# Optimization experiments

Measured on AMD Instinct MI355X. Metric: run time of the kernel, lower is better.

Reference implementation:

```python
import jax, jax.numpy as jnp
import numpy as np


def _axis_taps(g, size):
    # g: continuous grid coordinate; returns two neighbor indices (clamped)
    # and their linear interpolation weights, matching the HDRNet CUDA kernel:
    #   w = max(1 - |i + 0.5 - g|, 0)
    f = jnp.floor(g - 0.5)
    taps = []
    for off in (0.0, 1.0):
        idx = f + off
        w = jnp.maximum(1.0 - jnp.abs(idx + 0.5 - g), 0.0)
        i = jnp.clip(idx, 0, size - 1).astype(jnp.int32)
        taps.append((i, w))
    return taps


def bilateral_slice_apply(grid, guide, inp):
    # grid: [B, gh, gw, gd, n_out*(n_in+1)]   (has_offset=True)
    # guide: [B, H, W] in [0,1]
    # inp:  [B, H, W, n_in]
    B, gh, gw, gd, nc = grid.shape
    _, H, W, n_in = inp.shape
    n_out = nc // (n_in + 1)

    # continuous grid coords for each pixel / guide value
    gx = (jnp.arange(W, dtype=grid.dtype) + 0.5) * (gw / W)   # [W]
    gy = (jnp.arange(H, dtype=grid.dtype) + 0.5) * (gh / H)   # [H]
    gz = guide * gd                                           # [B,H,W]

    x_taps = _axis_taps(gx, gw)   # idx/w: [W]
    y_taps = _axis_taps(gy, gh)   # idx/w: [H]
    z_taps = _axis_taps(gz, gd)   # idx/w: [B,H,W]

    b = jnp.arange(B)[:, None, None]
    coeff = jnp.zeros((B, H, W, nc), dtype=grid.dtype)
    for yi, wy in y_taps:
        for xi, wx in x_taps:
            for zi, wz in z_taps:
                g = grid[b, yi[None, :, None], xi[None, None, :], zi]  # [B,H,W,nc]
                w = (wy[None, :, None] * wx[None, None, :] * wz)[..., None]
                coeff = coeff + w * g

    # per-pixel affine apply: out_o = sum_i A[o,i]*in_i + A[o,n_in]
    coeff = coeff.reshape(B, H, W, n_out, n_in + 1)
    out = jnp.einsum('bhwoc,bhwc->bhwo', coeff[..., :n_in], inp) + coeff[..., n_in]
    return out


def setup_inputs() -> dict:
    key = jax.random.key(0)
    k1, k2, k3 = jax.random.split(key, 3)
    B, gh, gw, gd = 4, 16, 16, 8
    H, W, n_in, n_out = 1024, 1024, 3, 3
    nc = n_out * (n_in + 1)  # has_offset=True -> 12
    grid = jax.random.normal(k1, (B, gh, gw, gd, nc), dtype=jnp.float32)
    guide = jax.random.uniform(k2, (B, H, W), dtype=jnp.float32)
    inp = jax.random.normal(k3, (B, H, W, n_in), dtype=jnp.float32)
    return {"grid": grid, "guide": guide, "input": inp}


def reference(grid, guide, input):
    return bilateral_slice_apply(grid, guide, input)
```

## Files before the change

### kernel.cpp

```cpp
#include <hip/hip_runtime.h>


__global__ __launch_bounds__(256) void BilateralSliceApply_kernel(
    const float* __restrict__ grid,
    const float* __restrict__ guide,
    const float* __restrict__ inp,
    float* __restrict__ out)
{
    __shared__ float4 lxi[3072];

    const int tx = blockIdx.x;
    const int ty = blockIdx.y;
    const int b  = blockIdx.z;
    const int t  = threadIdx.x;
    const int xl = t & 63;

    const int x0 = tx << 6;
    const int y0 = ty << 5;

    const int fy  = (ty == 0) ? -1 : ((ty - 1) >> 1);
    const int ycA = fy < 0 ? 0 : fy;
    const int ycB = (fy + 1 > 15) ? 15 : fy + 1;

    const int fx  = (xl < 32) ? (tx - 1) : tx;
    const int ix0 = fx < 0 ? 0 : fx;
    const int ix1 = (fx + 1 > 15) ? 15 : fx + 1;
    const float wx1 = ((float)(x0 + xl) + 0.5f) * 0.015625f - 0.5f - (float)fx;

    const int bbase = b << 4;
    for (int i = t >> 6; i < 48; i += 4) {
        const int z  = i & 7;
        const int w  = i >> 3;
        const int yc = (w >= 3) ? 1 : 0;
        const int c4 = w - yc * 3;
        const int ycell = yc ? ycB : ycA;
        const int cb = (bbase + ycell) << 4;
        const float* g0 = grid + ((size_t)(((cb + ix0) << 3) + z) * 12 + (c4 << 2));
        const float* g1 = grid + ((size_t)(((cb + ix1) << 3) + z) * 12 + (c4 << 2));
        const float4 a  = *(const float4*)g0;
        const float4 c  = *(const float4*)g1;
        float4 v;
        v.x = fmaf(wx1, c.x - a.x, a.x);
        v.y = fmaf(wx1, c.y - a.y, a.y);
        v.z = fmaf(wx1, c.z - a.z, a.z);
        v.w = fmaf(wx1, c.w - a.w, a.w);
        lxi[((((yc << 3) + z) * 3 + c4) << 6) + xl] = v;
    }
    __syncthreads();

    const int r0 = t >> 6;
#pragma unroll 2
    for (int k = 0; k < 8; ++k) {
        const int row = r0 + (k << 2);
        const int y   = y0 + row;
        const float wy1 = ((float)y + 0.5f) * 0.015625f - 0.5f - (float)fy;
        const float wy0 = 1.0f - wy1;
        const int pp = (((b << 10) + y) << 10) + x0 + xl;

        const float gz  = guide[pp] * 8.0f;
        const float fz  = floorf(gz - 0.5f);
        const float wz1 = gz - 0.5f - fz;
        const float wz0 = 1.0f - wz1;
        const int ifz = (int)fz;
        const int iz0 = ifz < 0 ? 0 : (ifz > 7 ? 7 : ifz);
        const int nz  = ifz + 1;
        const int iz1 = nz < 0 ? 0 : (nz > 7 ? 7 : nz);

        const float wA0 = wy0 * wz0, wA1 = wy0 * wz1;
        const float wB0 = wy1 * wz0, wB1 = wy1 * wz1;

        const int bA0 = ((iz0 * 3) << 6) + xl;
        const int bA1 = ((iz1 * 3) << 6) + xl;
        const int bB0 = (((8 + iz0) * 3) << 6) + xl;
        const int bB1 = (((8 + iz1) * 3) << 6) + xl;

        float4 cc[3];
#pragma unroll
        for (int c4 = 0; c4 < 3; ++c4) {
            const int o = c4 << 6;
            const float4 vA0 = lxi[bA0 + o];
            const float4 vA1 = lxi[bA1 + o];
            const float4 vB0 = lxi[bB0 + o];
            const float4 vB1 = lxi[bB1 + o];
            float4 v;
            v.x = fmaf(wA0, vA0.x, fmaf(wA1, vA1.x, fmaf(wB0, vB0.x, wB1 * vB1.x)));
            v.y = fmaf(wA0, vA0.y, fmaf(wA1, vA1.y, fmaf(wB0, vB0.y, wB1 * vB1.y)));
            v.z = fmaf(wA0, vA0.z, fmaf(wA1, vA1.z, fmaf(wB0, vB0.z, wB1 * vB1.z)));
            v.w = fmaf(wA0, vA0.w, fmaf(wA1, vA1.w, fmaf(wB0, vB0.w, wB1 * vB1.w)));
            cc[c4] = v;
        }

        const float in0 = inp[pp * 3 + 0];
        const float in1 = inp[pp * 3 + 1];
        const float in2 = inp[pp * 3 + 2];

        out[pp * 3 + 0] = fmaf(cc[0].x, in0, fmaf(cc[0].y, in1, fmaf(cc[0].z, in2, cc[0].w)));
        out[pp * 3 + 1] = fmaf(cc[1].x, in0, fmaf(cc[1].y, in1, fmaf(cc[1].z, in2, cc[1].w)));
        out[pp * 3 + 2] = fmaf(cc[2].x, in0, fmaf(cc[2].y, in1, fmaf(cc[2].z, in2, cc[2].w)));
    }
}

extern "C" void kernel_launch(void* const* d_in, const int* in_sizes, int n_in,
                              void* d_out, int out_size, void* d_ws, size_t ws_size,
                              hipStream_t stream) {
    const float* grid  = (const float*)d_in[0];
    const float* guide = (const float*)d_in[1];
    const float* inp   = (const float*)d_in[2];
    float* out = (float*)d_out;

    dim3 gridDim(16, 32, 4);
    BilateralSliceApply_kernel<<<gridDim, 256, 0, stream>>>(grid, guide, inp, out);
}
```

Measured before the change: 130.1 us.

## Store x-interpolated grid in fp16 shared memory and blend with packed half2 math

Stores the x-interpolated grid coefficients in shared memory as half2 pairs instead of float4, halving the LDS footprint and the bytes read per pixel. Each thread now loads all 12 channels per cell row in one pass, and the yz trilinear blend runs as packed half2 FMAs. Launch bounds now request 6 waves per SIMD and the unroll-2 pragma is removed. The tradeoff is reduced accuracy from fp16 storage and accumulation, which may exceed tolerance.

Measured after the change: 117.6 us. -9.6%, faster.

```diff
diff --git a/kernel.cpp b/kernel.cpp
--- a/kernel.cpp
+++ b/kernel.cpp
@@ -1,13 +1,18 @@
 #include <hip/hip_runtime.h>
+#include <hip/hip_fp16.h>
 
 
-__global__ __launch_bounds__(256) void BilateralSliceApply_kernel(
+struct __align__(16) H2x4 { __half2 x, y, z, w; };
+struct __align__(8)  H2x2 { __half2 a, b; };
+
+__global__ __launch_bounds__(256, 6) void BilateralSliceApply_kernel(
     const float* __restrict__ grid,
     const float* __restrict__ guide,
     const float* __restrict__ inp,
     float* __restrict__ out)
 {
-    __shared__ float4 lxi[3072];
+    __shared__ H2x4 lA[1024];
+    __shared__ H2x4 lB[512];
 
     const int tx = blockIdx.x;
     const int ty = blockIdx.y;
@@ -28,28 +33,50 @@
     const float wx1 = ((float)(x0 + xl) + 0.5f) * 0.015625f - 0.5f - (float)fx;
 
     const int bbase = b << 4;
-    for (int i = t >> 6; i < 48; i += 4) {
-        const int z  = i & 7;
-        const int w  = i >> 3;
-        const int yc = (w >= 3) ? 1 : 0;
-        const int c4 = w - yc * 3;
+    const int g0grp = t >> 6;
+#pragma unroll
+    for (int q = 0; q < 4; ++q) {
+        const int L  = g0grp + (q << 2);
+        const int yc = L >> 3;
+        const int z  = L & 7;
         const int ycell = yc ? ycB : ycA;
         const int cb = (bbase + ycell) << 4;
-        const float* g0 = grid + ((size_t)(((cb + ix0) << 3) + z) * 12 + (c4 << 2));
-        const float* g1 = grid + ((size_t)(((cb + ix1) << 3) + z) * 12 + (c4 << 2));
-        const float4 a  = *(const float4*)g0;
-        const float4 c  = *(const float4*)g1;
-        float4 v;
-        v.x = fmaf(wx1, c.x - a.x, a.x);
-        v.y = fmaf(wx1, c.y - a.y, a.y);
-        v.z = fmaf(wx1, c.z - a.z, a.z);
-        v.w = fmaf(wx1, c.w - a.w, a.w);
-        lxi[((((yc << 3) + z) * 3 + c4) << 6) + xl] = v;
+        const float* p0 = grid + (size_t)(((cb + ix0) << 3) + z) * 12;
+        const float* p1 = grid + (size_t)(((cb + ix1) << 3) + z) * 12;
+        const float4 a0 = *(const float4*)(p0 + 0);
+        const float4 a1 = *(const float4*)(p0 + 4);
+        const float4 a2 = *(const float4*)(p0 + 8);
+        const float4 b0 = *(const float4*)(p1 + 0);
+        const float4 b1 = *(const float4*)(p1 + 4);
+        const float4 b2 = *(const float4*)(p1 + 8);
+        const float v0  = fmaf(wx1, b0.x - a0.x, a0.x);
+        const float v1  = fmaf(wx1, b0.y - a0.y, a0.y);
+        const float v2  = fmaf(wx1, b0.z - a0.z, a0.z);
+        const float v3  = fmaf(wx1, b0.w - a0.w, a0.w);
+        const float v4  = fmaf(wx1, b1.x - a1.x, a1.x);
+        const float v5  = fmaf(wx1, b1.y - a1.y, a1.y);
+        const float v6  = fmaf(wx1, b1.z - a1.z, a1.z);
+        const float v7  = fmaf(wx1, b1.w - a1.w, a1.w);
+        const float v8  = fmaf(wx1, b2.x - a2.x, a2.x);
+        const float v9  = fmaf(wx1, b2.y - a2.y, a2.y);
+        const float v10 = fmaf(wx1, b2.z - a2.z, a2.z);
+        const float v11 = fmaf(wx1, b2.w - a2.w, a2.w);
+
+        H2x4 rowA;
+        rowA.x = __floats2half2_rn(v0, v1);
+        rowA.y = __floats2half2_rn(v2, v3);
+        rowA.z = __floats2half2_rn(v4, v5);
+        rowA.w = __floats2half2_rn(v6, v7);
+        lA[(L << 6) + xl] = rowA;
+
+        H2x2 rowB;
+        rowB.a = __floats2half2_rn(v8, v9);
+        rowB.b = __floats2half2_rn(v10, v11);
+        ((H2x2*)lB)[(((z << 6) + xl) << 1) + yc] = rowB;
     }
     __syncthreads();
 
     const int r0 = t >> 6;
-#pragma unroll 2
     for (int k = 0; k < 8; ++k) {
         const int row = r0 + (k << 2);
         const int y   = y0 + row;
@@ -66,37 +93,58 @@
         const int nz  = ifz + 1;
         const int iz1 = nz < 0 ? 0 : (nz > 7 ? 7 : nz);
 
-        const float wA0 = wy0 * wz0, wA1 = wy0 * wz1;
-        const float wB0 = wy1 * wz0, wB1 = wy1 * wz1;
+        const __half2 hA0 = __float2half2_rn(wy0 * wz0);
+        const __half2 hA1 = __float2half2_rn(wy0 * wz1);
+        const __half2 hB0 = __float2half2_rn(wy1 * wz0);
+        const __half2 hB1 = __float2half2_rn(wy1 * wz1);
 
-        const int bA0 = ((iz0 * 3) << 6) + xl;
-        const int bA1 = ((iz1 * 3) << 6) + xl;
-        const int bB0 = (((8 + iz0) * 3) << 6) + xl;
-        const int bB1 = (((8 + iz1) * 3) << 6) + xl;
+        const H2x4 vA00 = lA[(iz0 << 6) + xl];
+        const H2x4 vA01 = lA[(iz1 << 6) + xl];
+        const H2x4 vA10 = lA[((8 + iz0) << 6) + xl];
+        const H2x4 vA11 = lA[((8 + iz1) << 6) + xl];
+        const H2x4 vB0  = lB[(iz0 << 6) + xl];
+        const H2x4 vB1  = lB[(iz1 << 6) + xl];
 
-        float4 cc[3];
-#pragma unroll
-        for (int c4 = 0; c4 < 3; ++c4) {
-            const int o = c4 << 6;
-            const float4 vA0 = lxi[bA0 + o];
-            const float4 vA1 = lxi[bA1 + o];
-            const float4 vB0 = lxi[bB0 + o];
-            const float4 vB1 = lxi[bB1 + o];
-            float4 v;
-            v.x = fmaf(wA0, vA0.x, fmaf(wA1, vA1.x, fmaf(wB0, vB0.x, wB1 * vB1.x)));
-            v.y = fmaf(wA0, vA0.y, fmaf(wA1, vA1.y, fmaf(wB0, vB0.y, wB1 * vB1.y)));
-            v.z = fmaf(wA0, vA0.z, fmaf(wA1, vA1.z, fmaf(wB0, vB0.z, wB1 * vB1.z)));
-            v.w = fmaf(wA0, vA0.w, fmaf(wA1, vA1.w, fmaf(wB0, vB0.w, wB1 * vB1.w)));
-            cc[c4] = v;
-        }
+        __half2 q0 = __hmul2(hA0, vA00.x);
+        __half2 q1 = __hmul2(hA0, vA00.y);
+        __half2 q2 = __hmul2(hA0, vA00.z);
+        __half2 q3 = __hmul2(hA0, vA00.w);
+        q0 = __hfma2(hA1, vA01.x, q0);
+        q1 = __hfma2(hA1, vA01.y, q1);
+        q2 = __hfma2(hA1, vA01.z, q2);
+        q3 = __hfma2(hA1, vA01.w, q3);
+        q0 = __hfma2(hB0, vA10.x, q0);
+        q1 = __hfma2(hB0, vA10.y, q1);
+        q2 = __hfma2(hB0, vA10.z, q2);
+        q3 = __hfma2(hB0, vA10.w, q3);
+        q0 = __hfma2(hB1, vA11.x, q0);
+        q1 = __hfma2(hB1, vA11.y, q1);
+        q2 = __hfma2(hB1, vA11.z, q2);
+        q3 = __hfma2(hB1, vA11.w, q3);
 
-        const float in0 = inp[pp * 3 + 0];
-        const float in1 = inp[pp * 3 + 1];
-        const float in2 = inp[pp * 3 + 2];
+        __half2 q4 = __hmul2(hA0, vB0.x);
+        __half2 q5 = __hmul2(hA0, vB0.y);
+        q4 = __hfma2(hA1, vB1.x, q4);
+        q5 = __hfma2(hA1, vB1.y, q5);
+        q4 = __hfma2(hB0, vB0.z, q4);
+        q5 = __hfma2(hB0, vB0.w, q5);
+        q4 = __hfma2(hB1, vB1.z, q4);
+        q5 = __hfma2(hB1, vB1.w, q5);
 
-        out[pp * 3 + 0] = fmaf(cc[0].x, in0, fmaf(cc[0].y, in1, fmaf(cc[0].z, in2, cc[0].w)));
-        out[pp * 3 + 1] = fmaf(cc[1].x, in0, fmaf(cc[1].y, in1, fmaf(cc[1].z, in2, cc[1].w)));
-        out[pp * 3 + 2] = fmaf(cc[2].x, in0, fmaf(cc[2].y, in1, fmaf(cc[2].z, in2, cc[2].w)));
+        const float c0  = __low2float(q0),  c1  = __high2float(q0);
+        const float c2  = __low2float(q1),  c3  = __high2float(q1);
+        const float c4  = __low2float(q2),  c5  = __high2float(q2);
+        const float c6  = __low2float(q3),  c7  = __high2float(q3);
+        const float c8  = __low2float(q4),  c9  = __high2float(q4);
+        const float c10 = __low2float(q5),  c11 = __high2float(q5);
+
+        const float in0 = inp[(size_t)pp * 3 + 0];
+        const float in1 = inp[(size_t)pp * 3 + 1];
+        const float in2 = inp[(size_t)pp * 3 + 2];
+
+        out[(size_t)pp * 3 + 0] = fmaf(c0, in0, fmaf(c1,  in1, fmaf(c2,  in2, c3)));
+        out[(size_t)pp * 3 + 1] = fmaf(c4, in0, fmaf(c5,  in1, fmaf(c6,  in2, c7)));
+        out[(size_t)pp * 3 + 2] = fmaf(c8, in0, fmaf(c9,  in1, fmaf(c10, in2, c11)));
     }
 }
 
```
